# Kernel optimization log

Hardware: AMD Instinct MI355X
Metric: run time of the kernel (lower is better)

## Reference

```python
import jax, jax.numpy as jnp
import numpy as np

NEG_SLOPE = 0.2
RECON_W = 0.1
BN_EPS = 1e-5


def gat_conv(x, edge_index, W, a_src, a_dst, b):
    """PyG-style GATConv (eval mode, add_self_loops=True, concat heads).
    x: [N, F_in], W: [F_in, H*C], a_src/a_dst: [H, C], b: [H*C]."""
    N = x.shape[0]
    H, C = a_src.shape
    h = (x @ W).reshape(N, H, C)                      # [N,H,C]
    loop = jnp.arange(N, dtype=edge_index.dtype)
    src = jnp.concatenate([edge_index[0], loop])
    dst = jnp.concatenate([edge_index[1], loop])
    alpha_src = jnp.sum(h * a_src, axis=-1)           # [N,H]
    alpha_dst = jnp.sum(h * a_dst, axis=-1)           # [N,H]
    e = jax.nn.leaky_relu(alpha_src[src] + alpha_dst[dst], NEG_SLOPE)  # [E,H]
    # segment softmax over incoming edges of each destination node
    m = jax.ops.segment_max(e, dst, num_segments=N)
    e = jnp.exp(e - m[dst])
    s = jax.ops.segment_sum(e, dst, num_segments=N)
    p = e / s[dst]                                    # [E,H]
    out = jax.ops.segment_sum(p[:, :, None] * h[src], dst, num_segments=N)  # [N,H,C]
    return out.reshape(N, H * C) + b


def setup_inputs() -> dict:
    key = jax.random.key(0)
    ks = jax.random.split(key, 24)
    N, E = 100000, 800000
    F_in, hid, heads, n_cls, ctx_d, expl_d = 128, 32, 4, 10, 6, 32
    HC = hid * heads  # 128
    g = lambda k, shp, sc=0.1: jax.random.normal(k, shp, dtype=jnp.float32) * sc
    return {
        "x": jax.random.normal(ks[0], (N, F_in), dtype=jnp.float32),
        "edge_index": jax.random.randint(ks[1], (2, E), 0, N, dtype=jnp.int32),
        "context": jax.random.normal(ks[2], (N, ctx_d), dtype=jnp.float32),
        # GATConv 1: F_in -> hid, heads
        "W1": g(ks[3], (F_in, HC)), "a_src1": g(ks[4], (heads, hid)),
        "a_dst1": g(ks[5], (heads, hid)), "b1": g(ks[6], (HC,)),
        # BatchNorm1d(HC), eval mode
        "bn_gamma": jnp.ones((HC,), jnp.float32), "bn_beta": g(ks[7], (HC,)),
        "bn_mean": g(ks[8], (HC,)), "bn_var": jax.random.uniform(ks[9], (HC,), jnp.float32, 0.5, 1.5),
        # GATConv 2: HC -> hid, 1 head
        "W2": g(ks[10], (HC, hid)), "a_src2": g(ks[11], (1, hid)),
        "a_dst2": g(ks[12], (1, hid)), "b2": g(ks[13], (hid,)),
        # Reasoner MLP: ctx_d -> hid -> expl_d
        "rw1": g(ks[14], (ctx_d, hid)), "rb1": g(ks[15], (hid,)),
        "rw2": g(ks[16], (hid, expl_d)), "rb2": g(ks[17], (expl_d,)),
        # Decoder: expl_d -> hid
        "dw": g(ks[18], (expl_d, hid)), "db": g(ks[19], (hid,)),
        # Classifier: hid -> n_cls
        "cw": g(ks[20], (hid, n_cls)), "cb": g(ks[21], (n_cls,)),
    }


def reference(x, edge_index, context, W1, a_src1, a_dst1, b1,
              bn_gamma, bn_beta, bn_mean, bn_var,
              W2, a_src2, a_dst2, b2, rw1, rb1, rw2, rb2, dw, db, cw, cb):
    # layer 1: GAT -> BN(eval) -> ELU (dropout inactive in eval)
    h = gat_conv(x, edge_index, W1, a_src1, a_dst1, b1)
    h = (h - bn_mean) * jax.lax.rsqrt(bn_var + BN_EPS) * bn_gamma + bn_beta
    h = jax.nn.elu(h)
    # layer 2: GAT (1 head)
    h = gat_conv(h, edge_index, W2, a_src2, a_dst2, b2)  # [N, hid]
    # reasoner + decoder
    expl = jnp.maximum(context @ rw1 + rb1, 0.0) @ rw2 + rb2   # [N, expl_d]
    recon = expl @ dw + db                                     # [N, hid]
    combined = h + RECON_W * recon
    logits = combined @ cw + cb
    return jax.nn.log_softmax(logits, axis=1), expl
```

## Files before the change

### kernel.cpp

```cpp
#include <hip/hip_runtime.h>
#include <hip/hip_bf16.h>
#include <math.h>

#define NEG_SLOPE 0.2f
#define RECON_W 0.1f
#define BN_EPS 1e-5f
#define CAP 64
#define NB_SCAT 256

typedef __attribute__((ext_vector_type(8))) short short8;
typedef __attribute__((ext_vector_type(4))) float f32x4;

__device__ __forceinline__ float lrelu(float v) {
    return (v >= 0.f) ? v : NEG_SLOPE * v;
}
__device__ __forceinline__ unsigned short f2bf(float f) {
    unsigned int u = __float_as_uint(f);
    u = (u + 0x7fffu + ((u >> 16) & 1u)) >> 16;
    return (unsigned short)u;
}
__device__ __forceinline__ float bf2f(unsigned short u) {
    return __uint_as_float(((unsigned int)u) << 16);
}
__device__ __forceinline__ unsigned int pack2bf(float a, float b) {
    return (unsigned int)f2bf(a) | ((unsigned int)f2bf(b) << 16);
}
__device__ __forceinline__ void unpack2(unsigned int u, float& a, float& b) {
    a = bf2f((unsigned short)u);
    b = bf2f((unsigned short)(u >> 16));
}

__global__ __launch_bounds__(256) void prep_kernel(
    const float* __restrict__ W1, const float* __restrict__ W2,
    const float* __restrict__ b1, const float* __restrict__ g,
    const float* __restrict__ be, const float* __restrict__ m, const float* __restrict__ v,
    unsigned short* __restrict__ w1t, unsigned short* __restrict__ w2t,
    float* __restrict__ bnsc, float* __restrict__ bnsh) {
    int b = blockIdx.x, tid = threadIdx.x;
    if (b < 64) {
        int e = b * 256 + tid;
        w1t[e] = f2bf(W1[(e & 127) * 128 + (e >> 7)]);
    } else {
        #pragma unroll
        for (int it = 0; it < 16; it++) {
            int e = it * 256 + tid;
            w2t[e] = f2bf(W2[(e & 127) * 32 + (e >> 7)]);
        }
        if (tid < 128) {
            float s = rsqrtf(v[tid] + BN_EPS) * g[tid];
            bnsc[tid] = s;
            bnsh[tid] = (b1[tid] - m[tid]) * s + be[tid];
        }
    }
}

__global__ __launch_bounds__(256) void gemm1_mfma_kernel(
    const float* __restrict__ x, const unsigned short* __restrict__ w1t,
    const float* __restrict__ a_src, const float* __restrict__ a_dst,
    unsigned short* __restrict__ h1g, float* __restrict__ as1, float* __restrict__ ad1, int N,
    const int* __restrict__ esrc, const int* __restrict__ edst, int E,
    int* __restrict__ cnt, int* __restrict__ csrS) {
    __shared__ unsigned short sA[64 * 128];
    __shared__ unsigned short sBt[128 * 128];
    __shared__ float s_as[128], s_ad[128];
    int tid = threadIdx.x;

    if (blockIdx.x < NB_SCAT) {
        int stride = NB_SCAT * 256;
        #pragma unroll 2
        for (int e = blockIdx.x * 256 + tid; e < E; e += stride) {
            int s = esrc[e], d = edst[e];
            int pos = atomicAdd(&cnt[d], 1);
            if (pos < CAP) csrS[(size_t)d * CAP + pos] = s;
        }
        return;
    }
    int rowBase = (blockIdx.x - NB_SCAT) * 64;

    if (tid < 128) { s_as[tid] = a_src[tid]; s_ad[tid] = a_dst[tid]; }
    #pragma unroll
    for (int u = 0; u < 8; u++) {
        int f = tid + u * 256;
        int r = f >> 5, cg = f & 31;
        int gr = rowBase + r;
        float4 vv = make_float4(0.f, 0.f, 0.f, 0.f);
        if (gr < N) vv = *(const float4*)(x + (size_t)gr * 128 + cg * 4);
        uint2 pk;
        pk.x = pack2bf(vv.x, vv.y);
        pk.y = pack2bf(vv.z, vv.w);
        ((uint2*)sA)[f] = pk;
    }
    #pragma unroll
    for (int u = 0; u < 8; u++) {
        int f = tid + u * 256;
        ((uint4*)sBt)[f] = ((const uint4*)w1t)[f];
    }
    __syncthreads();

    int lane = tid & 63;
    int w = tid >> 6;
    int quad = lane >> 4;
    int m16 = lane & 15;

    f32x4 acc[8];
    #pragma unroll
    for (int t = 0; t < 8; t++) acc[t] = (f32x4){0.f, 0.f, 0.f, 0.f};

    #pragma unroll
    for (int kc = 0; kc < 4; kc++) {
        int k0 = kc * 32 + quad * 8;
        short8 af = *(const short8*)(sA + ((w * 16 + m16) * 128 + k0));
        #pragma unroll
        for (int t = 0; t < 8; t++) {
            short8 bf = *(const short8*)(sBt + ((t * 16 + m16) * 128 + k0));
            acc[t] = __builtin_amdgcn_mfma_f32_16x16x32_bf16(af, bf, acc[t], 0, 0, 0);
        }
    }

    #pragma unroll
    for (int t = 0; t < 8; t++) {
        #pragma unroll
        for (int r = 0; r < 4; r++) {
            int row = w * 16 + quad * 4 + r;
            int col = t * 16 + m16;
            sA[row * 128 + col] = f2bf(acc[t][r]);
        }
    }
    __syncthreads();
    #pragma unroll
    for (int u = 0; u < 8; u++) {
        int f = tid + u * 256;
        int r = f >> 5, cg = f & 31;
        int gr = rowBase + r;
        if (gr < N) *(uint2*)(h1g + (size_t)gr * 128 + cg * 4) = ((const uint2*)sA)[f];
    }
    {
        int row = tid >> 2, head = tid & 3;
        int gr = rowBase + row;
        if (gr < N) {
            const unsigned int* rowp = (const unsigned int*)(sA + row * 128);
            float ps = 0.f, pd = 0.f;
            #pragma unroll
            for (int j = 0; j < 16; j++) {
                float f0, f1;
                unpack2(rowp[head * 16 + j], f0, f1);
                int c = head * 32 + j * 2;
                ps = fmaf(f0, s_as[c], fmaf(f1, s_as[c + 1], ps));
                pd = fmaf(f0, s_ad[c], fmaf(f1, s_ad[c + 1], pd));
            }
            as1[gr * 4 + head] = ps;
            ad1[gr * 4 + head] = pd;
        }
    }
}

__global__ __launch_bounds__(256) void agg1_kernel(
    const unsigned short* __restrict__ h1g,
    const float* __restrict__ as1, const float* __restrict__ ad1,
    const int* __restrict__ cnt, const int* __restrict__ csrS,
    const float* __restrict__ bnscale, const float* __restrict__ bnshift,
    unsigned short* __restrict__ h1p, int N) {
    __shared__ int   sSrc[16][CAP + 1];
    __shared__ float sW[16][CAP + 1][4];
    int tid = threadIdx.x;
    int nid = tid >> 4;
    int l   = tid & 15;
    int n = blockIdx.x * 16 + nid;
    bool alive = (n < N);
    int total = 0;

    if (alive) {
        int deg = min(cnt[n], CAP);
        total = deg + 1;
        float4 ad4 = *(const float4*)(ad1 + (size_t)n * 4);
        for (int slot = l; slot < total; slot += 16) {
            int s = (slot < deg) ? csrS[(size_t)n * CAP + slot] : n;
            sSrc[nid][slot] = s;
            float4 a = *(const float4*)(as1 + (size_t)s * 4);
            float4 w4;
            w4.x = __expf(lrelu(a.x + ad4.x));
            w4.y = __expf(lrelu(a.y + ad4.y));
            w4.z = __expf(lrelu(a.z + ad4.z));
            w4.w = __expf(lrelu(a.w + ad4.w));
            *(float4*)(&sW[nid][slot][0]) = w4;
        }
    }
    __syncthreads();
    if (!alive) return;

    int hl = l >> 2;
    unsigned choff = (unsigned)(l << 3);
    const int* sS = sSrc[nid];
    const float* sWp = &sW[nid][0][0];

    float pa0 = 0.f, pa1 = 0.f, pa2 = 0.f, pa3 = 0.f;
    float pa4 = 0.f, pa5 = 0.f, pa6 = 0.f, pa7 = 0.f;
    float pb0 = 0.f, pb1 = 0.f, pb2 = 0.f, pb3 = 0.f;
    float pb4 = 0.f, pb5 = 0.f, pb6 = 0.f, pb7 = 0.f;
    float sa = 0.f, sb = 0.f;
    int j = 0;
    for (; j + 1 < total; j += 2) {
        int s0 = sS[j];
        int s1 = sS[j + 1];
        float w0 = sWp[(j << 2) + hl];
        float w1 = sWp[((j + 1) << 2) + hl];
        uint4 u0 = *(const uint4*)(h1g + (((unsigned)s0 << 7) + choff));
        uint4 u1 = *(const uint4*)(h1g + (((unsigned)s1 << 7) + choff));
        float f0, f1;
        unpack2(u0.x, f0, f1); pa0 = fmaf(w0, f0, pa0); pa1 = fmaf(w0, f1, pa1);
        unpack2(u0.y, f0, f1); pa2 = fmaf(w0, f0, pa2); pa3 = fmaf(w0, f1, pa3);
        unpack2(u0.z, f0, f1); pa4 = fmaf(w0, f0, pa4); pa5 = fmaf(w0, f1, pa5);
        unpack2(u0.w, f0, f1); pa6 = fmaf(w0, f0, pa6); pa7 = fmaf(w0, f1, pa7);
        sa += w0;
        unpack2(u1.x, f0, f1); pb0 = fmaf(w1, f0, pb0); pb1 = fmaf(w1, f1, pb1);
        unpack2(u1.y, f0, f1); pb2 = fmaf(w1, f0, pb2); pb3 = fmaf(w1, f1, pb3);
        unpack2(u1.z, f0, f1); pb4 = fmaf(w1, f0, pb4); pb5 = fmaf(w1, f1, pb5);
        unpack2(u1.w, f0, f1); pb6 = fmaf(w1, f0, pb6); pb7 = fmaf(w1, f1, pb7);
        sb += w1;
    }
    if (j < total) {
        int s0 = sS[j];
        float w0 = sWp[(j << 2) + hl];
        uint4 u0 = *(const uint4*)(h1g + (((unsigned)s0 << 7) + choff));
        float f0, f1;
        unpack2(u0.x, f0, f1); pa0 = fmaf(w0, f0, pa0); pa1 = fmaf(w0, f1, pa1);
        unpack2(u0.y, f0, f1); pa2 = fmaf(w0, f0, pa2); pa3 = fmaf(w0, f1, pa3);
        unpack2(u0.z, f0, f1); pa4 = fmaf(w0, f0, pa4); pa5 = fmaf(w0, f1, pa5);
        unpack2(u0.w, f0, f1); pa6 = fmaf(w0, f0, pa6); pa7 = fmaf(w0, f1, pa7);
        sa += w0;
    }
    float inv = 1.f / (sa + sb);
    float4 sc0 = *(const float4*)(bnscale + l * 8);
    float4 sc1 = *(const float4*)(bnscale + l * 8 + 4);
    float4 sh0 = *(const float4*)(bnshift + l * 8);
    float4 sh1 = *(const float4*)(bnshift + l * 8 + 4);
    float o0 = fmaf((pa0 + pb0) * inv, sc0.x, sh0.x);
    float o1 = fmaf((pa1 + pb1) * inv, sc0.y, sh0.y);
    float o2 = fmaf((pa2 + pb2) * inv, sc0.z, sh0.z);
    float o3 = fmaf((pa3 + pb3) * inv, sc0.w, sh0.w);
    float o4 = fmaf((pa4 + pb4) * inv, sc1.x, sh1.x);
    float o5 = fmaf((pa5 + pb5) * inv, sc1.y, sh1.y);
    float o6 = fmaf((pa6 + pb6) * inv, sc1.z, sh1.z);
    float o7 = fmaf((pa7 + pb7) * inv, sc1.w, sh1.w);
    o0 = (o0 > 0.f) ? o0 : expm1f(o0);
    o1 = (o1 > 0.f) ? o1 : expm1f(o1);
    o2 = (o2 > 0.f) ? o2 : expm1f(o2);
    o3 = (o3 > 0.f) ? o3 : expm1f(o3);
    o4 = (o4 > 0.f) ? o4 : expm1f(o4);
    o5 = (o5 > 0.f) ? o5 : expm1f(o5);
    o6 = (o6 > 0.f) ? o6 : expm1f(o6);
    o7 = (o7 > 0.f) ? o7 : expm1f(o7);
    uint4 pk;
    pk.x = pack2bf(o0, o1);
    pk.y = pack2bf(o2, o3);
    pk.z = pack2bf(o4, o5);
    pk.w = pack2bf(o6, o7);
    *(uint4*)(h1p + (size_t)n * 128 + l * 8) = pk;
}

__global__ __launch_bounds__(256) void gemm2_mfma_kernel(
    const unsigned short* __restrict__ A, const unsigned short* __restrict__ w2t,
    const float* __restrict__ a_src, const float* __restrict__ a_dst,
    unsigned short* __restrict__ h2g, float* __restrict__ as2, float* __restrict__ ad2, int N) {
    __shared__ unsigned short sA[64 * 128];
    __shared__ unsigned short sBt[32 * 128];
    __shared__ unsigned short sC[64 * 32];
    __shared__ float s_as[32], s_ad[32];
    int tid = threadIdx.x;
    int rowBase = blockIdx.x * 64;

    if (tid < 32) { s_as[tid] = a_src[tid]; s_ad[tid] = a_dst[tid]; }
    #pragma unroll
    for (int u = 0; u < 4; u++) {
        int f = tid + u * 256;
        int r = f >> 4, g = f & 15;
        int gr = rowBase + r;
        uint4 vv = make_uint4(0, 0, 0, 0);
        if (gr < N) vv = *(const uint4*)(A + (size_t)gr * 128 + g * 8);
        ((uint4*)sA)[f] = vv;
    }
    #pragma unroll
    for (int u = 0; u < 2; u++) {
        int f = tid + u * 256;
        ((uint4*)sBt)[f] = ((const uint4*)w2t)[f];
    }
    __syncthreads();

    int lane = tid & 63;
    int w = tid >> 6;
    int quad = lane >> 4;
    int m16 = lane & 15;

    f32x4 acc[2];
    acc[0] = (f32x4){0.f, 0.f, 0.f, 0.f};
    acc[1] = (f32x4){0.f, 0.f, 0.f, 0.f};
    #pragma unroll
    for (int kc = 0; kc < 4; kc++) {
        int k0 = kc * 32 + quad * 8;
        short8 af = *(const short8*)(sA + ((w * 16 + m16) * 128 + k0));
        #pragma unroll
        for (int t = 0; t < 2; t++) {
            short8 bf = *(const short8*)(sBt + ((t * 16 + m16) * 128 + k0));
            acc[t] = __builtin_amdgcn_mfma_f32_16x16x32_bf16(af, bf, acc[t], 0, 0, 0);
        }
    }
    #pragma unroll
    for (int t = 0; t < 2; t++) {
        #pragma unroll
        for (int r = 0; r < 4; r++) {
            int row = w * 16 + quad * 4 + r;
            sC[row * 32 + t * 16 + m16] = f2bf(acc[t][r]);
        }
    }
    __syncthreads();
    {
        int r = tid >> 2, g = tid & 3;
        int gr = rowBase + r;
        if (gr < N) *(uint4*)(h2g + (size_t)gr * 32 + g * 8) = ((const uint4*)sC)[tid];
    }
    if (tid < 64) {
        int gr = rowBase + tid;
        if (gr < N) {
            const unsigned int* rowp = (const unsigned int*)(sC + tid * 32);
            float ps = 0.f, pd = 0.f;
            #pragma unroll
            for (int j = 0; j < 16; j++) {
                float f0, f1;
                unpack2(rowp[j], f0, f1);
                ps = fmaf(f0, s_as[j * 2], fmaf(f1, s_as[j * 2 + 1], ps));
                pd = fmaf(f0, s_ad[j * 2], fmaf(f1, s_ad[j * 2 + 1], pd));
            }
            as2[gr] = ps;
            ad2[gr] = pd;
        }
    }
}

__global__ __launch_bounds__(256) void agg2_kernel(
    const unsigned short* __restrict__ h2g,
    const float* __restrict__ as2, const float* __restrict__ ad2,
    const int* __restrict__ cnt, const int* __restrict__ csrS,
    const float* __restrict__ b2, float* __restrict__ hl2, int N) {
    __shared__ int   sSrc[32][CAP + 1];
    __shared__ float sW[32][CAP + 1];
    int tid = threadIdx.x;
    int nid = tid >> 3;
    int l   = tid & 7;
    int n = blockIdx.x * 32 + nid;
    bool alive = (n < N);
    int total = 0;

    if (alive) {
        int deg = min(cnt[n], CAP);
        total = deg + 1;
        float ad = ad2[n];
        for (int slot = l; slot < total; slot += 8) {
            int s = (slot < deg) ? csrS[(size_t)n * CAP + slot] : n;
            sSrc[nid][slot] = s;
            sW[nid][slot] = __expf(lrelu(as2[s] + ad));
        }
    }
    __syncthreads();
    if (!alive) return;

    unsigned choff = (unsigned)(l << 2);
    const int* sS = sSrc[nid];
    const float* sWp = sW[nid];

    float a0a = 0.f, a1a = 0.f, a2a = 0.f, a3a = 0.f, sa = 0.f;
    float a0b = 0.f, a1b = 0.f, a2b = 0.f, a3b = 0.f, sb = 0.f;
    int j = 0;
    for (; j + 1 < total; j += 2) {
        int s0 = sS[j];
        int s1 = sS[j + 1];
        float w0 = sWp[j];
        float w1 = sWp[j + 1];
        uint2 u0 = *(const uint2*)(h2g + (((unsigned)s0 << 5) + choff));
        uint2 u1 = *(const uint2*)(h2g + (((unsigned)s1 << 5) + choff));
        float f0, f1;
        unpack2(u0.x, f0, f1); a0a = fmaf(w0, f0, a0a); a1a = fmaf(w0, f1, a1a);
        unpack2(u0.y, f0, f1); a2a = fmaf(w0, f0, a2a); a3a = fmaf(w0, f1, a3a);
        sa += w0;
        unpack2(u1.x, f0, f1); a0b = fmaf(w1, f0, a0b); a1b = fmaf(w1, f1, a1b);
        unpack2(u1.y, f0, f1); a2b = fmaf(w1, f0, a2b); a3b = fmaf(w1, f1, a3b);
        sb += w1;
    }
    if (j < total) {
        int s0 = sS[j];
        float w0 = sWp[j];
        uint2 u0 = *(const uint2*)(h2g + (((unsigned)s0 << 5) + choff));
        float f0, f1;
        unpack2(u0.x, f0, f1); a0a = fmaf(w0, f0, a0a); a1a = fmaf(w0, f1, a1a);
        unpack2(u0.y, f0, f1); a2a = fmaf(w0, f0, a2a); a3a = fmaf(w0, f1, a3a);
        sa += w0;
    }
    float inv = 1.f / (sa + sb);
    float4 bb = *(const float4*)(b2 + l * 4);
    float4 o;
    o.x = (a0a + a0b) * inv + bb.x;
    o.y = (a1a + a1b) * inv + bb.y;
    o.z = (a2a + a2b) * inv + bb.z;
    o.w = (a3a + a3b) * inv + bb.w;
    *(float4*)(hl2 + (size_t)n * 32 + l * 4) = o;
}

__global__ __launch_bounds__(256) void head_kernel(
    const float* __restrict__ context, const float* __restrict__ hl2,
    const float* __restrict__ rw1, const float* __restrict__ rb1,
    const float* __restrict__ rw2, const float* __restrict__ rb2,
    const float* __restrict__ dw, const float* __restrict__ db,
    const float* __restrict__ cw, const float* __restrict__ cb,
    float* __restrict__ out_lsm, float* __restrict__ out_expl, int N) {
    __shared__ float s_rw1[192], s_rw2[1024], s_dw[1024], s_cw[320];
    __shared__ float s_rb1[32], s_rb2[32], s_db[32], s_cb[10];
    int tid = threadIdx.x;
    for (int i = tid; i < 192; i += 256) s_rw1[i] = rw1[i];
    for (int i = tid; i < 1024; i += 256) { s_rw2[i] = rw2[i]; s_dw[i] = dw[i]; }
    for (int i = tid; i < 320; i += 256) s_cw[i] = cw[i];
    if (tid < 32) { s_rb1[tid] = rb1[tid]; s_rb2[tid] = rb2[tid]; s_db[tid] = db[tid]; }
    if (tid < 10) s_cb[tid] = cb[tid];
    __syncthreads();
    int n = blockIdx.x * 256 + tid;
    if (n >= N) return;

    float ctx[6];
    #pragma unroll
    for (int i = 0; i < 6; i++) ctx[i] = context[(size_t)n * 6 + i];

    float t1[32];
    #pragma unroll
    for (int c = 0; c < 32; c++) t1[c] = s_rb1[c];
    #pragma unroll
    for (int i = 0; i < 6; i++) {
        float s = ctx[i];
        #pragma unroll
        for (int c = 0; c < 32; c++) t1[c] = fmaf(s, s_rw1[i * 32 + c], t1[c]);
    }
    #pragma unroll
    for (int c = 0; c < 32; c++) t1[c] = fmaxf(t1[c], 0.f);

    float ex[32];
    #pragma unroll
    for (int c = 0; c < 32; c++) ex[c] = s_rb2[c];
    #pragma unroll
    for (int c = 0; c < 32; c++) {
        float s = t1[c];
        #pragma unroll
        for (int c2 = 0; c2 < 32; c2++) ex[c2] = fmaf(s, s_rw2[c * 32 + c2], ex[c2]);
    }
    #pragma unroll
    for (int c = 0; c < 32; c += 4)
        *(float4*)(out_expl + (size_t)n * 32 + c) = make_float4(ex[c], ex[c + 1], ex[c + 2], ex[c + 3]);

    float rec[32];
    #pragma unroll
    for (int k = 0; k < 32; k++) rec[k] = s_db[k];
    #pragma unroll
    for (int c = 0; c < 32; c++) {
        float s = ex[c];
        #pragma unroll
        for (int k = 0; k < 32; k++) rec[k] = fmaf(s, s_dw[c * 32 + k], rec[k]);
    }
    float comb[32];
    #pragma unroll
    for (int k = 0; k < 32; k += 4) {
        float4 h = *(const float4*)(hl2 + (size_t)n * 32 + k);
        comb[k] = h.x + RECON_W * rec[k];
        comb[k + 1] = h.y + RECON_W * rec[k + 1];
        comb[k + 2] = h.z + RECON_W * rec[k + 2];
        comb[k + 3] = h.w + RECON_W * rec[k + 3];
    }
    float lg[10];
    #pragma unroll
    for (int j = 0; j < 10; j++) lg[j] = s_cb[j];
    #pragma unroll
    for (int k = 0; k < 32; k++) {
        float s = comb[k];
        #pragma unroll
        for (int j = 0; j < 10; j++) lg[j] = fmaf(s, s_cw[k * 10 + j], lg[j]);
    }
    float mx = lg[0];
    #pragma unroll
    for (int j = 1; j < 10; j++) mx = fmaxf(mx, lg[j]);
    float se = 0.f;
    #pragma unroll
    for (int j = 0; j < 10; j++) se += expf(lg[j] - mx);
    float lse = mx + logf(se);
    #pragma unroll
    for (int j = 0; j < 10; j++) out_lsm[(size_t)n * 10 + j] = lg[j] - lse;
}

extern "C" void kernel_launch(void* const* d_in, const int* in_sizes, int n_in,
                              void* d_out, int out_size, void* d_ws, size_t ws_size,
                              hipStream_t stream) {
    const float* x    = (const float*)d_in[0];
    const int* ei     = (const int*)d_in[1];
    const float* ctx  = (const float*)d_in[2];
    const float* W1   = (const float*)d_in[3];
    const float* a_s1 = (const float*)d_in[4];
    const float* a_d1 = (const float*)d_in[5];
    const float* b1   = (const float*)d_in[6];
    const float* bn_g = (const float*)d_in[7];
    const float* bn_b = (const float*)d_in[8];
    const float* bn_m = (const float*)d_in[9];
    const float* bn_v = (const float*)d_in[10];
    const float* W2   = (const float*)d_in[11];
    const float* a_s2 = (const float*)d_in[12];
    const float* a_d2 = (const float*)d_in[13];
    const float* b2   = (const float*)d_in[14];
    const float* rw1  = (const float*)d_in[15];
    const float* rb1  = (const float*)d_in[16];
    const float* rw2  = (const float*)d_in[17];
    const float* rb2  = (const float*)d_in[18];
    const float* dw   = (const float*)d_in[19];
    const float* db   = (const float*)d_in[20];
    const float* cw   = (const float*)d_in[21];
    const float* cb   = (const float*)d_in[22];

    int N = in_sizes[0] / 128;
    int E = in_sizes[1] / 2;
    const int* esrc = ei;
    const int* edst = ei + E;

    char* w = (char*)d_ws;
    auto alloc = [&](size_t bytes) {
        void* p = (void*)w;
        w += (bytes + 255) & ~(size_t)255;
        return p;
    };
    unsigned short* h1g = (unsigned short*)alloc((size_t)N * 128 * 2);
    unsigned short* h1p = (unsigned short*)alloc((size_t)N * 128 * 2);
    float* as1  = (float*)alloc((size_t)N * 4 * 4);
    float* ad1  = (float*)alloc((size_t)N * 4 * 4);
    float* as2  = (float*)alloc((size_t)N * 4);
    float* ad2  = (float*)alloc((size_t)N * 4);
    int* cnt    = (int*)alloc((size_t)N * 4);
    int* csrS   = (int*)alloc((size_t)N * CAP * 4);
    float* bnsc = (float*)alloc(128 * 4);
    float* bnsh = (float*)alloc(128 * 4);
    unsigned short* w1t = (unsigned short*)alloc(128 * 128 * 2);
    unsigned short* w2t = (unsigned short*)alloc(32 * 128 * 2);
    unsigned short* h2g = h1g;
    float* hl2 = (float*)(h1g + (size_t)N * 32);

    float* out0 = (float*)d_out;
    float* out1 = out0 + (size_t)N * 10;

    hipMemsetAsync(cnt, 0, (size_t)N * 4, stream);

    prep_kernel<<<65, 256, 0, stream>>>(W1, W2, b1, bn_g, bn_b, bn_m, bn_v,
                                        w1t, w2t, bnsc, bnsh);
    gemm1_mfma_kernel<<<NB_SCAT + (N + 63) / 64, 256, 0, stream>>>(
        x, w1t, a_s1, a_d1, h1g, as1, ad1, N, esrc, edst, E, cnt, csrS);
    agg1_kernel<<<(N + 15) / 16, 256, 0, stream>>>(h1g, as1, ad1, cnt, csrS,
                                                   bnsc, bnsh, h1p, N);
    gemm2_mfma_kernel<<<(N + 63) / 64, 256, 0, stream>>>(h1p, w2t, a_s2, a_d2, h2g, as2, ad2, N);
    agg2_kernel<<<(N + 31) / 32, 256, 0, stream>>>(h2g, as2, ad2, cnt, csrS, b2, hl2, N);
    head_kernel<<<(N + 255) / 256, 256, 0, stream>>>(ctx, hl2, rw1, rb1, rw2, rb2,
                                                     dw, db, cw, cb, out0, out1, N);
}
```

Baseline: 289.2 us.

## Fuse layer-1 aggregation with GEMM2 and layer-2 aggregation with MLP head

Merges agg1 and gemm2 into one kernel, so each block of 16 nodes computes its aggregated, BN+ELU'd features into shared memory and runs the 128->32 MFMA projection right away. This removes the h1p round trip through global memory. It also fuses agg2 with the reasoner/decoder/classifier head, keeping the layer-2 output in shared memory and splitting the head MLP across 8 lanes per node with a shuffle reduction. The cost is per-block reloads of W2 and the head weights, extra barriers, and only one wave doing the small MFMA while the other waves sit idle.

```diff
diff --git a/kernel.cpp b/kernel.cpp
--- a/kernel.cpp
+++ b/kernel.cpp
@@ -154,20 +154,27 @@
     }
 }
 
-__global__ __launch_bounds__(256) void agg1_kernel(
+__global__ __launch_bounds__(256) void agg1_gemm2_kernel(
     const unsigned short* __restrict__ h1g,
     const float* __restrict__ as1, const float* __restrict__ ad1,
     const int* __restrict__ cnt, const int* __restrict__ csrS,
     const float* __restrict__ bnscale, const float* __restrict__ bnshift,
-    unsigned short* __restrict__ h1p, int N) {
+    const unsigned short* __restrict__ w2t,
+    const float* __restrict__ a_src2, const float* __restrict__ a_dst2,
+    unsigned short* __restrict__ h2g, float* __restrict__ as2, float* __restrict__ ad2,
+    int N) {
     __shared__ int   sSrc[16][CAP + 1];
-    __shared__ float sW[16][CAP + 1][4];
+    __shared__ __align__(16) float sW[16][CAP + 1][4];
+    __shared__ unsigned short sH[16 * 128];
+    __shared__ float s_as[32], s_ad[32];
     int tid = threadIdx.x;
     int nid = tid >> 4;
     int l   = tid & 15;
     int n = blockIdx.x * 16 + nid;
     bool alive = (n < N);
     int total = 0;
+
+    if (tid < 32) { s_as[tid] = a_src2[tid]; s_ad[tid] = a_dst2[tid]; }
 
     if (alive) {
         int deg = min(cnt[n], CAP);
@@ -186,7 +193,6 @@
         }
     }
     __syncthreads();
-    if (!alive) return;
 
     int hl = l >> 2;
     unsigned choff = (unsigned)(l << 3);
@@ -229,106 +235,85 @@
         unpack2(u0.w, f0, f1); pa6 = fmaf(w0, f0, pa6); pa7 = fmaf(w0, f1, pa7);
         sa += w0;
     }
-    float inv = 1.f / (sa + sb);
-    float4 sc0 = *(const float4*)(bnscale + l * 8);
-    float4 sc1 = *(const float4*)(bnscale + l * 8 + 4);
-    float4 sh0 = *(const float4*)(bnshift + l * 8);
-    float4 sh1 = *(const float4*)(bnshift + l * 8 + 4);
-    float o0 = fmaf((pa0 + pb0) * inv, sc0.x, sh0.x);
-    float o1 = fmaf((pa1 + pb1) * inv, sc0.y, sh0.y);
-    float o2 = fmaf((pa2 + pb2) * inv, sc0.z, sh0.z);
-    float o3 = fmaf((pa3 + pb3) * inv, sc0.w, sh0.w);
-    float o4 = fmaf((pa4 + pb4) * inv, sc1.x, sh1.x);
-    float o5 = fmaf((pa5 + pb5) * inv, sc1.y, sh1.y);
-    float o6 = fmaf((pa6 + pb6) * inv, sc1.z, sh1.z);
-    float o7 = fmaf((pa7 + pb7) * inv, sc1.w, sh1.w);
-    o0 = (o0 > 0.f) ? o0 : expm1f(o0);
-    o1 = (o1 > 0.f) ? o1 : expm1f(o1);
-    o2 = (o2 > 0.f) ? o2 : expm1f(o2);
-    o3 = (o3 > 0.f) ? o3 : expm1f(o3);
-    o4 = (o4 > 0.f) ? o4 : expm1f(o4);
-    o5 = (o5 > 0.f) ? o5 : expm1f(o5);
-    o6 = (o6 > 0.f) ? o6 : expm1f(o6);
-    o7 = (o7 > 0.f) ? o7 : expm1f(o7);
-    uint4 pk;
-    pk.x = pack2bf(o0, o1);
-    pk.y = pack2bf(o2, o3);
-    pk.z = pack2bf(o4, o5);
-    pk.w = pack2bf(o6, o7);
-    *(uint4*)(h1p + (size_t)n * 128 + l * 8) = pk;
-}
-
-__global__ __launch_bounds__(256) void gemm2_mfma_kernel(
-    const unsigned short* __restrict__ A, const unsigned short* __restrict__ w2t,
-    const float* __restrict__ a_src, const float* __restrict__ a_dst,
-    unsigned short* __restrict__ h2g, float* __restrict__ as2, float* __restrict__ ad2, int N) {
-    __shared__ unsigned short sA[64 * 128];
-    __shared__ unsigned short sBt[32 * 128];
-    __shared__ unsigned short sC[64 * 32];
-    __shared__ float s_as[32], s_ad[32];
-    int tid = threadIdx.x;
-    int rowBase = blockIdx.x * 64;
-
-    if (tid < 32) { s_as[tid] = a_src[tid]; s_ad[tid] = a_dst[tid]; }
-    #pragma unroll
-    for (int u = 0; u < 4; u++) {
-        int f = tid + u * 256;
-        int r = f >> 4, g = f & 15;
-        int gr = rowBase + r;
-        uint4 vv = make_uint4(0, 0, 0, 0);
-        if (gr < N) vv = *(const uint4*)(A + (size_t)gr * 128 + g * 8);
-        ((uint4*)sA)[f] = vv;
-    }
-    #pragma unroll
-    for (int u = 0; u < 2; u++) {
-        int f = tid + u * 256;
-        ((uint4*)sBt)[f] = ((const uint4*)w2t)[f];
-    }
-    __syncthreads();
-
-    int lane = tid & 63;
-    int w = tid >> 6;
-    int quad = lane >> 4;
-    int m16 = lane & 15;
-
-    f32x4 acc[2];
-    acc[0] = (f32x4){0.f, 0.f, 0.f, 0.f};
-    acc[1] = (f32x4){0.f, 0.f, 0.f, 0.f};
-    #pragma unroll
-    for (int kc = 0; kc < 4; kc++) {
-        int k0 = kc * 32 + quad * 8;
-        short8 af = *(const short8*)(sA + ((w * 16 + m16) * 128 + k0));
+    uint4 pk = make_uint4(0u, 0u, 0u, 0u);
+    if (alive) {
+        float inv = 1.f / (sa + sb);
+        float4 sc0 = *(const float4*)(bnscale + l * 8);
+        float4 sc1 = *(const float4*)(bnscale + l * 8 + 4);
+        float4 sh0 = *(const float4*)(bnshift + l * 8);
+        float4 sh1 = *(const float4*)(bnshift + l * 8 + 4);
+        float o0 = fmaf((pa0 + pb0) * inv, sc0.x, sh0.x);
+        float o1 = fmaf((pa1 + pb1) * inv, sc0.y, sh0.y);
+        float o2 = fmaf((pa2 + pb2) * inv, sc0.z, sh0.z);
+        float o3 = fmaf((pa3 + pb3) * inv, sc0.w, sh0.w);
+        float o4 = fmaf((pa4 + pb4) * inv, sc1.x, sh1.x);
+        float o5 = fmaf((pa5 + pb5) * inv, sc1.y, sh1.y);
+        float o6 = fmaf((pa6 + pb6) * inv, sc1.z, sh1.z);
+        float o7 = fmaf((pa7 + pb7) * inv, sc1.w, sh1.w);
+        o0 = (o0 > 0.f) ? o0 : expm1f(o0);
+        o1 = (o1 > 0.f) ? o1 : expm1f(o1);
+        o2 = (o2 > 0.f) ? o2 : expm1f(o2);
+        o3 = (o3 > 0.f) ? o3 : expm1f(o3);
+        o4 = (o4 > 0.f) ? o4 : expm1f(o4);
+        o5 = (o5 > 0.f) ? o5 : expm1f(o5);
+        o6 = (o6 > 0.f) ? o6 : expm1f(o6);
+        o7 = (o7 > 0.f) ? o7 : expm1f(o7);
+        pk.x = pack2bf(o0, o1);
+        pk.y = pack2bf(o2, o3);
+        pk.z = pack2bf(o4, o5);
+        pk.w = pack2bf(o6, o7);
+    }
+    *(uint4*)(sH + nid * 128 + l * 8) = pk;
+    __syncthreads();
+
+    unsigned short* sBt = (unsigned short*)&sW[0][0][0];
+    unsigned short* sC  = sBt + 32 * 128;
+    #pragma unroll
+    for (int u = 0; u < 2; u++) ((uint4*)sBt)[tid + u * 256] = ((const uint4*)w2t)[tid + u * 256];
+    __syncthreads();
+
+    if (tid < 64) {
+        int quad = tid >> 4, m16 = tid & 15;
+        f32x4 acc2[2];
+        acc2[0] = (f32x4){0.f, 0.f, 0.f, 0.f};
+        acc2[1] = (f32x4){0.f, 0.f, 0.f, 0.f};
+        #pragma unroll
+        for (int kc = 0; kc < 4; kc++) {
+            int k0 = kc * 32 + quad * 8;
+            short8 af = *(const short8*)(sH + m16 * 128 + k0);
+            #pragma unroll
+            for (int t = 0; t < 2; t++) {
+                short8 bf = *(const short8*)(sBt + (t * 16 + m16) * 128 + k0);
+                acc2[t] = __builtin_amdgcn_mfma_f32_16x16x32_bf16(af, bf, acc2[t], 0, 0, 0);
+            }
+        }
         #pragma unroll
         for (int t = 0; t < 2; t++) {
-            short8 bf = *(const short8*)(sBt + ((t * 16 + m16) * 128 + k0));
-            acc[t] = __builtin_amdgcn_mfma_f32_16x16x32_bf16(af, bf, acc[t], 0, 0, 0);
-        }
-    }
-    #pragma unroll
-    for (int t = 0; t < 2; t++) {
-        #pragma unroll
-        for (int r = 0; r < 4; r++) {
-            int row = w * 16 + quad * 4 + r;
-            sC[row * 32 + t * 16 + m16] = f2bf(acc[t][r]);
-        }
-    }
-    __syncthreads();
-    {
-        int r = tid >> 2, g = tid & 3;
-        int gr = rowBase + r;
+            #pragma unroll
+            for (int r = 0; r < 4; r++) {
+                sC[(quad * 4 + r) * 32 + t * 16 + m16] = f2bf(acc2[t][r]);
+            }
+        }
+    }
+    __syncthreads();
+
+    if (tid < 64) {
+        int row = tid >> 2, g = tid & 3;
+        int gr = blockIdx.x * 16 + row;
         if (gr < N) *(uint4*)(h2g + (size_t)gr * 32 + g * 8) = ((const uint4*)sC)[tid];
     }
-    if (tid < 64) {
-        int gr = rowBase + tid;
+    if (tid >= 64 && tid < 80) {
+        int row = tid - 64;
+        int gr = blockIdx.x * 16 + row;
         if (gr < N) {
-            const unsigned int* rowp = (const unsigned int*)(sC + tid * 32);
+            const unsigned int* rowp = (const unsigned int*)(sC + row * 32);
             float ps = 0.f, pd = 0.f;
             #pragma unroll
-            for (int j = 0; j < 16; j++) {
+            for (int jj = 0; jj < 16; jj++) {
                 float f0, f1;
-                unpack2(rowp[j], f0, f1);
-                ps = fmaf(f0, s_as[j * 2], fmaf(f1, s_as[j * 2 + 1], ps));
-                pd = fmaf(f0, s_ad[j * 2], fmaf(f1, s_ad[j * 2 + 1], pd));
+                unpack2(rowp[jj], f0, f1);
+                ps = fmaf(f0, s_as[jj * 2], fmaf(f1, s_as[jj * 2 + 1], ps));
+                pd = fmaf(f0, s_ad[jj * 2], fmaf(f1, s_ad[jj * 2 + 1], pd));
             }
             as2[gr] = ps;
             ad2[gr] = pd;
@@ -336,14 +321,28 @@
     }
 }
 
-__global__ __launch_bounds__(256) void agg2_kernel(
+__global__ __launch_bounds__(256) void agg2_head_kernel(
     const unsigned short* __restrict__ h2g,
     const float* __restrict__ as2, const float* __restrict__ ad2,
     const int* __restrict__ cnt, const int* __restrict__ csrS,
-    const float* __restrict__ b2, float* __restrict__ hl2, int N) {
+    const float* __restrict__ b2, const float* __restrict__ context,
+    const float* __restrict__ rw1, const float* __restrict__ rb1,
+    const float* __restrict__ rw2, const float* __restrict__ rb2,
+    const float* __restrict__ dw, const float* __restrict__ db,
+    const float* __restrict__ cw, const float* __restrict__ cb,
+    float* __restrict__ out_lsm, float* __restrict__ out_expl, int N) {
     __shared__ int   sSrc[32][CAP + 1];
-    __shared__ float sW[32][CAP + 1];
+    __shared__ __align__(16) float sW[32][CAP + 1];
+    __shared__ float sHL[32][32];
+    __shared__ float s_rw1[192], s_rw2[1024], s_dw[1024], s_cw[320];
+    __shared__ float s_rb1[32], s_rb2[32], s_db[32], s_b2[32], s_cb[16];
     int tid = threadIdx.x;
+    for (int i = tid; i < 1024; i += 256) { s_rw2[i] = rw2[i]; s_dw[i] = dw[i]; }
+    for (int i = tid; i < 320; i += 256) s_cw[i] = cw[i];
+    if (tid < 192) s_rw1[tid] = rw1[tid];
+    if (tid < 32) { s_rb1[tid] = rb1[tid]; s_rb2[tid] = rb2[tid]; s_db[tid] = db[tid]; s_b2[tid] = b2[tid]; }
+    if (tid < 10) s_cb[tid] = cb[tid];
+
     int nid = tid >> 3;
     int l   = tid & 7;
     int n = blockIdx.x * 32 + nid;
@@ -361,11 +360,10 @@
         }
     }
     __syncthreads();
-    if (!alive) return;
 
     unsigned choff = (unsigned)(l << 2);
     const int* sS = sSrc[nid];
-    const float* sWp = sW[nid];
+    const float* sWp = &sW[nid][0];
 
     float a0a = 0.f, a1a = 0.f, a2a = 0.f, a3a = 0.f, sa = 0.f;
     float a0b = 0.f, a1b = 0.f, a2b = 0.f, a3b = 0.f, sb = 0.f;
@@ -394,100 +392,93 @@
         unpack2(u0.y, f0, f1); a2a = fmaf(w0, f0, a2a); a3a = fmaf(w0, f1, a3a);
         sa += w0;
     }
-    float inv = 1.f / (sa + sb);
-    float4 bb = *(const float4*)(b2 + l * 4);
-    float4 o;
-    o.x = (a0a + a0b) * inv + bb.x;
-    o.y = (a1a + a1b) * inv + bb.y;
-    o.z = (a2a + a2b) * inv + bb.z;
-    o.w = (a3a + a3b) * inv + bb.w;
-    *(float4*)(hl2 + (size_t)n * 32 + l * 4) = o;
-}
-
-__global__ __launch_bounds__(256) void head_kernel(
-    const float* __restrict__ context, const float* __restrict__ hl2,
-    const float* __restrict__ rw1, const float* __restrict__ rb1,
-    const float* __restrict__ rw2, const float* __restrict__ rb2,
-    const float* __restrict__ dw, const float* __restrict__ db,
-    const float* __restrict__ cw, const float* __restrict__ cb,
-    float* __restrict__ out_lsm, float* __restrict__ out_expl, int N) {
-    __shared__ float s_rw1[192], s_rw2[1024], s_dw[1024], s_cw[320];
-    __shared__ float s_rb1[32], s_rb2[32], s_db[32], s_cb[10];
-    int tid = threadIdx.x;
-    for (int i = tid; i < 192; i += 256) s_rw1[i] = rw1[i];
-    for (int i = tid; i < 1024; i += 256) { s_rw2[i] = rw2[i]; s_dw[i] = dw[i]; }
-    for (int i = tid; i < 320; i += 256) s_cw[i] = cw[i];
-    if (tid < 32) { s_rb1[tid] = rb1[tid]; s_rb2[tid] = rb2[tid]; s_db[tid] = db[tid]; }
-    if (tid < 10) s_cb[tid] = cb[tid];
-    __syncthreads();
-    int n = blockIdx.x * 256 + tid;
-    if (n >= N) return;
-
-    float ctx[6];
-    #pragma unroll
-    for (int i = 0; i < 6; i++) ctx[i] = context[(size_t)n * 6 + i];
-
-    float t1[32];
-    #pragma unroll
-    for (int c = 0; c < 32; c++) t1[c] = s_rb1[c];
-    #pragma unroll
-    for (int i = 0; i < 6; i++) {
-        float s = ctx[i];
-        #pragma unroll
-        for (int c = 0; c < 32; c++) t1[c] = fmaf(s, s_rw1[i * 32 + c], t1[c]);
-    }
-    #pragma unroll
-    for (int c = 0; c < 32; c++) t1[c] = fmaxf(t1[c], 0.f);
-
-    float ex[32];
-    #pragma unroll
-    for (int c = 0; c < 32; c++) ex[c] = s_rb2[c];
-    #pragma unroll
-    for (int c = 0; c < 32; c++) {
-        float s = t1[c];
-        #pragma unroll
-        for (int c2 = 0; c2 < 32; c2++) ex[c2] = fmaf(s, s_rw2[c * 32 + c2], ex[c2]);
-    }
-    #pragma unroll
-    for (int c = 0; c < 32; c += 4)
-        *(float4*)(out_expl + (size_t)n * 32 + c) = make_float4(ex[c], ex[c + 1], ex[c + 2], ex[c + 3]);
-
-    float rec[32];
-    #pragma unroll
-    for (int k = 0; k < 32; k++) rec[k] = s_db[k];
-    #pragma unroll
-    for (int c = 0; c < 32; c++) {
-        float s = ex[c];
-        #pragma unroll
-        for (int k = 0; k < 32; k++) rec[k] = fmaf(s, s_dw[c * 32 + k], rec[k]);
-    }
-    float comb[32];
-    #pragma unroll
-    for (int k = 0; k < 32; k += 4) {
-        float4 h = *(const float4*)(hl2 + (size_t)n * 32 + k);
-        comb[k] = h.x + RECON_W * rec[k];
-        comb[k + 1] = h.y + RECON_W * rec[k + 1];
-        comb[k + 2] = h.z + RECON_W * rec[k + 2];
-        comb[k + 3] = h.w + RECON_W * rec[k + 3];
-    }
-    float lg[10];
-    #pragma unroll
-    for (int j = 0; j < 10; j++) lg[j] = s_cb[j];
-    #pragma unroll
-    for (int k = 0; k < 32; k++) {
-        float s = comb[k];
-        #pragma unroll
-        for (int j = 0; j < 10; j++) lg[j] = fmaf(s, s_cw[k * 10 + j], lg[j]);
-    }
-    float mx = lg[0];
-    #pragma unroll
-    for (int j = 1; j < 10; j++) mx = fmaxf(mx, lg[j]);
-    float se = 0.f;
-    #pragma unroll
-    for (int j = 0; j < 10; j++) se += expf(lg[j] - mx);
-    float lse = mx + logf(se);
-    #pragma unroll
-    for (int j = 0; j < 10; j++) out_lsm[(size_t)n * 10 + j] = lg[j] - lse;
+    if (alive) {
+        float inv = 1.f / (sa + sb);
+        int c0 = l * 4;
+        sHL[nid][c0 + 0] = (a0a + a0b) * inv + s_b2[c0 + 0];
+        sHL[nid][c0 + 1] = (a1a + a1b) * inv + s_b2[c0 + 1];
+        sHL[nid][c0 + 2] = (a2a + a2b) * inv + s_b2[c0 + 2];
+        sHL[nid][c0 + 3] = (a3a + a3b) * inv + s_b2[c0 + 3];
+    }
+    __syncthreads();
+
+    float* sEX = &sW[0][0];
+
+    if (alive) {
+        int c0 = l * 4;
+        float ctxv[6];
+        #pragma unroll
+        for (int i = 0; i < 6; i++) ctxv[i] = context[(size_t)n * 6 + i];
+        float t1[32];
+        #pragma unroll
+        for (int c = 0; c < 32; c++) t1[c] = s_rb1[c];
+        #pragma unroll
+        for (int i = 0; i < 6; i++) {
+            float s = ctxv[i];
+            #pragma unroll
+            for (int c = 0; c < 32; c++) t1[c] = fmaf(s, s_rw1[i * 32 + c], t1[c]);
+        }
+        #pragma unroll
+        for (int c = 0; c < 32; c++) t1[c] = fmaxf(t1[c], 0.f);
+
+        float e0 = s_rb2[c0], e1 = s_rb2[c0 + 1], e2 = s_rb2[c0 + 2], e3 = s_rb2[c0 + 3];
+        #pragma unroll
+        for (int c = 0; c < 32; c++) {
+            float s = t1[c];
+            const float* rp = s_rw2 + c * 32 + c0;
+            e0 = fmaf(s, rp[0], e0); e1 = fmaf(s, rp[1], e1);
+            e2 = fmaf(s, rp[2], e2); e3 = fmaf(s, rp[3], e3);
+        }
+        *(float4*)(out_expl + (size_t)n * 32 + c0) = make_float4(e0, e1, e2, e3);
+        sEX[nid * 32 + c0 + 0] = e0;
+        sEX[nid * 32 + c0 + 1] = e1;
+        sEX[nid * 32 + c0 + 2] = e2;
+        sEX[nid * 32 + c0 + 3] = e3;
+    }
+    __syncthreads();
+
+    if (alive) {
+        int c0 = l * 4;
+        float r0 = s_db[c0], r1 = s_db[c0 + 1], r2 = s_db[c0 + 2], r3 = s_db[c0 + 3];
+        #pragma unroll
+        for (int c = 0; c < 32; c++) {
+            float s = sEX[nid * 32 + c];
+            const float* dp = s_dw + c * 32 + c0;
+            r0 = fmaf(s, dp[0], r0); r1 = fmaf(s, dp[1], r1);
+            r2 = fmaf(s, dp[2], r2); r3 = fmaf(s, dp[3], r3);
+        }
+        float cmb[4];
+        cmb[0] = sHL[nid][c0 + 0] + RECON_W * r0;
+        cmb[1] = sHL[nid][c0 + 1] + RECON_W * r1;
+        cmb[2] = sHL[nid][c0 + 2] + RECON_W * r2;
+        cmb[3] = sHL[nid][c0 + 3] + RECON_W * r3;
+        float lg[10];
+        #pragma unroll
+        for (int c = 0; c < 10; c++) lg[c] = 0.f;
+        #pragma unroll
+        for (int k = 0; k < 4; k++) {
+            float s = cmb[k];
+            const float* cp = s_cw + (c0 + k) * 10;
+            #pragma unroll
+            for (int c = 0; c < 10; c++) lg[c] = fmaf(s, cp[c], lg[c]);
+        }
+        #pragma unroll
+        for (int m = 1; m < 8; m <<= 1) {
+            #pragma unroll
+            for (int c = 0; c < 10; c++) lg[c] += __shfl_xor(lg[c], m);
+        }
+        #pragma unroll
+        for (int c = 0; c < 10; c++) lg[c] += s_cb[c];
+        float mx = lg[0];
+        #pragma unroll
+        for (int c = 1; c < 10; c++) mx = fmaxf(mx, lg[c]);
+        float se = 0.f;
+        #pragma unroll
+        for (int c = 0; c < 10; c++) se += expf(lg[c] - mx);
+        float lse = mx + logf(se);
+        out_lsm[(size_t)n * 10 + l] = lg[l] - lse;
+        if (l < 2) out_lsm[(size_t)n * 10 + 8 + l] = lg[8 + l] - lse;
+    }
 }
 
 extern "C" void kernel_launch(void* const* d_in, const int* in_sizes, int n_in,
@@ -529,7 +520,7 @@
         return p;
     };
     unsigned short* h1g = (unsigned short*)alloc((size_t)N * 128 * 2);
-    unsigned short* h1p = (unsigned short*)alloc((size_t)N * 128 * 2);
+    unsigned short* h2g = (unsigned short*)alloc((size_t)N * 32 * 2);
     float* as1  = (float*)alloc((size_t)N * 4 * 4);
     float* ad1  = (float*)alloc((size_t)N * 4 * 4);
     float* as2  = (float*)alloc((size_t)N * 4);
@@ -540,8 +531,6 @@
     float* bnsh = (float*)alloc(128 * 4);
     unsigned short* w1t = (unsigned short*)alloc(128 * 128 * 2);
     unsigned short* w2t = (unsigned short*)alloc(32 * 128 * 2);
-    unsigned short* h2g = h1g;
-    float* hl2 = (float*)(h1g + (size_t)N * 32);
 
     float* out0 = (float*)d_out;
     float* out1 = out0 + (size_t)N * 10;
@@ -552,10 +541,9 @@
                                         w1t, w2t, bnsc, bnsh);
     gemm1_mfma_kernel<<<NB_SCAT + (N + 63) / 64, 256, 0, stream>>>(
         x, w1t, a_s1, a_d1, h1g, as1, ad1, N, esrc, edst, E, cnt, csrS);
-    agg1_kernel<<<(N + 15) / 16, 256, 0, stream>>>(h1g, as1, ad1, cnt, csrS,
-                                                   bnsc, bnsh, h1p, N);
-    gemm2_mfma_kernel<<<(N + 63) / 64, 256, 0, stream>>>(h1p, w2t, a_s2, a_d2, h2g, as2, ad2, N);
-    agg2_kernel<<<(N + 31) / 32, 256, 0, stream>>>(h2g, as2, ad2, cnt, csrS, b2, hl2, N);
-    head_kernel<<<(N + 255) / 256, 256, 0, stream>>>(ctx, hl2, rw1, rb1, rw2, rb2,
-                                                     dw, db, cw, cb, out0, out1, N);
-}
+    agg1_gemm2_kernel<<<(N + 15) / 16, 256, 0, stream>>>(
+        h1g, as1, ad1, cnt, csrS, bnsc, bnsh, w2t, a_s2, a_d2, h2g, as2, ad2, N);
+    agg2_head_kernel<<<(N + 31) / 32, 256, 0, stream>>>(
+        h2g, as2, ad2, cnt, csrS, b2, ctx, rw1, rb1, rw2, rb2,
+        dw, db, cw, cb, out0, out1, N);
+}
```

After: 272.5 us. -5.8%, faster.
